# Kernel optimization log

Measured on AMD Instinct MI355X. Metric: run time of the kernel, lower is better.

The kernel has to match this reference:

```python
import jax, jax.numpy as jnp
import numpy as np

DIM = 1024
HEADS = 16
HEAD_DIM = 64
ROT = 32          # rotary_emb_dim = min(max(head_dim//2, 32), head_dim)
BASE = 10000.0
SEQ = 2048
BATCH = 2


def setup_inputs() -> dict:
    key = jax.random.key(0)
    k1, k2, k3, k4 = jax.random.split(key, 4)
    s = 0.02
    return {
        "x": jax.random.normal(k1, (BATCH, SEQ, DIM), dtype=jnp.float32),
        # Linear weights stored as [in, out] (equivalent to torch W^T)
        "w_q": jax.random.normal(k2, (DIM, HEADS * HEAD_DIM), dtype=jnp.float32) * s,
        "w_kv": jax.random.normal(k3, (DIM, 2 * HEADS * HEAD_DIM), dtype=jnp.float32) * s,
        "w_out": jax.random.normal(k4, (HEADS * HEAD_DIM, DIM), dtype=jnp.float32) * s,
    }


def _rotate_half(t):
    # x-transformers style: split last dim in half, (-x2, x1)
    x1, x2 = t[..., : ROT // 2], t[..., ROT // 2 :]
    return jnp.concatenate([-x2, x1], axis=-1)


def _apply_rope(t, cos, sin):
    # rotate only the first ROT dims of head_dim, pass through the rest
    t_rot, t_pass = t[..., :ROT], t[..., ROT:]
    t_rot = t_rot * cos + _rotate_half(t_rot) * sin
    return jnp.concatenate([t_rot, t_pass], axis=-1)


def reference(x, w_q, w_kv, w_out):
    b, n, _ = x.shape
    # QKV projections
    q = (x @ w_q).reshape(b, n, HEADS, HEAD_DIM).transpose(0, 2, 1, 3)  # b h n d
    k, v = jnp.split(x @ w_kv, 2, axis=-1)
    k = k.reshape(b, n, HEADS, HEAD_DIM).transpose(0, 2, 1, 3)
    v = v.reshape(b, n, HEADS, HEAD_DIM).transpose(0, 2, 1, 3)

    # rotary embedding over full kv length (no cache -> k.shape[-2] == n)
    inv_freq = 1.0 / (BASE ** (jnp.arange(0, ROT, 2, dtype=jnp.float32) / ROT))
    freqs = jnp.arange(n, dtype=jnp.float32)[:, None] * inv_freq[None, :]  # [n, ROT/2]
    freqs = jnp.concatenate([freqs, freqs], axis=-1)                        # [n, ROT]
    cos, sin = jnp.cos(freqs), jnp.sin(freqs)
    q = _apply_rope(q, cos, sin)
    k = _apply_rope(k, cos, sin)

    # causal attention
    scale = HEAD_DIM ** -0.5
    scores = jnp.einsum('bhid,bhjd->bhij', q, k) * scale  # [b,h,n,n]
    causal_mask = jnp.tril(jnp.ones((n, n), dtype=bool))
    scores = jnp.where(causal_mask, scores, jnp.finfo(scores.dtype).min)
    attn = jax.nn.softmax(scores, axis=-1)
    out = jnp.einsum('bhij,bhjd->bhid', attn, v)

    out = out.transpose(0, 2, 1, 3).reshape(b, n, HEADS * HEAD_DIM)
    return out @ w_out
```

## Files before the change

kernel.cpp:

```cpp
#include <hip/hip_runtime.h>

typedef unsigned short u16;
typedef unsigned int u32;
typedef __bf16 bf16x8 __attribute__((ext_vector_type(8)));
typedef unsigned short u16x8v __attribute__((ext_vector_type(8)));
typedef unsigned short u16x4v __attribute__((ext_vector_type(4)));
typedef unsigned int u32x4 __attribute__((ext_vector_type(4)));
typedef float f32x4 __attribute__((ext_vector_type(4)));
typedef float f32x16 __attribute__((ext_vector_type(16)));

#define SEQ 2048
#define NH 16
#define HD 64
#define DIMM 1024

__device__ __forceinline__ u16 f2bf(float f) {
  unsigned u = __builtin_bit_cast(unsigned, f);
  u += 0x7fffu + ((u >> 16) & 1u);
  return (u16)(u >> 16);
}
__device__ __forceinline__ float bf2f(u16 b) {
  return __builtin_bit_cast(float, ((unsigned)b) << 16);
}
__device__ __forceinline__ u32 pk2(float a, float b) {
  return (u32)f2bf(a) | ((u32)f2bf(b) << 16);
}

__device__ __forceinline__ void gload16(const u16* g, u16* l) {
  __builtin_amdgcn_global_load_lds(
      (const __attribute__((address_space(1))) unsigned int*)g,
      (__attribute__((address_space(3))) unsigned int*)l, 16, 0, 0);
}

__global__ void conv_x(const float* __restrict__ x, u16* __restrict__ oh) {
  size_t i = (size_t)blockIdx.x * 256 + threadIdx.x;
  f32x4 v = *(const f32x4*)(x + i * 4);
  u16x4v h;
#pragma unroll
  for (int j = 0; j < 4; ++j) h[j] = f2bf(v[j]);
  *(u16x4v*)(oh + i * 4) = h;
}

__global__ void conv_wT(const float* __restrict__ W, u16* __restrict__ Wt,
                        int Kd, int Nd) {
  __shared__ float t[32][33];
  int n0 = blockIdx.x * 32, k0 = blockIdx.y * 32;
  int c = threadIdx.x & 31, r8 = threadIdx.x >> 5;
#pragma unroll
  for (int rr = 0; rr < 32; rr += 8)
    t[r8 + rr][c] = W[(size_t)(k0 + r8 + rr) * Nd + n0 + c];
  __syncthreads();
#pragma unroll
  for (int rr = 0; rr < 32; rr += 8)
    Wt[(size_t)(n0 + r8 + rr) * Kd + k0 + c] = f2bf(t[c][r8 + rr]);
}

__global__ void __launch_bounds__(256, 2)
gemmQKV(const u16* __restrict__ Ah, const u16* __restrict__ Bt,
        u16* __restrict__ Qb, u16* __restrict__ Kb, u16* __restrict__ Vb,
        int M, int N, int K) {
  __shared__ u16 AsH[128][64];
  __shared__ u16 BsH[128][64];
  const int tid = threadIdx.x;
  const int lane = tid & 63, wave = tid >> 6;
  const int wr = wave >> 1, wc = wave & 1;
  const int lr = lane & 15, lg = lane >> 4;
  const int bm = blockIdx.y * 128, bn = blockIdx.x * 128;
  const int lrow = lane >> 3;
  const int lcol8 = (lane & 7) * 8;

  f32x4 acc[4][4];
#pragma unroll
  for (int m = 0; m < 4; ++m)
#pragma unroll
    for (int n = 0; n < 4; ++n) acc[m][n] = (f32x4){0.f, 0.f, 0.f, 0.f};

  for (int k0 = 0; k0 < K; k0 += 64) {
    __syncthreads();
#pragma unroll
    for (int c = 0; c < 4; ++c) {
      int r0 = wave * 32 + c * 8;
      size_t arow = (size_t)(bm + r0 + lrow) * K + k0 + lcol8;
      size_t brow = (size_t)(bn + r0 + lrow) * K + k0 + lcol8;
      gload16(Ah + arow, &AsH[r0][0]);
      gload16(Bt + brow, &BsH[r0][0]);
    }
    __syncthreads();
#pragma unroll
    for (int kk = 0; kk < 2; ++kk) {
      bf16x8 afh[4], bfh[4];
#pragma unroll
      for (int m = 0; m < 4; ++m)
        afh[m] = *(const bf16x8*)&AsH[wr * 64 + m * 16 + lr][kk * 32 + lg * 8];
#pragma unroll
      for (int n = 0; n < 4; ++n)
        bfh[n] = *(const bf16x8*)&BsH[wc * 64 + n * 16 + lr][kk * 32 + lg * 8];
#pragma unroll
      for (int m = 0; m < 4; ++m)
#pragma unroll
        for (int n = 0; n < 4; ++n)
          acc[m][n] = __builtin_amdgcn_mfma_f32_16x16x32_bf16(afh[m], bfh[n],
                                                              acc[m][n], 0, 0, 0);
    }
  }

  const int sel = bn >> 10;
  u16* __restrict__ dst = sel == 0 ? Qb : (sel == 1 ? Kb : Vb);
  if (sel < 2) {
    float inv = __expf(-(float)lr * 0.5756462732485115f);
#pragma unroll
    for (int m = 0; m < 4; ++m) {
#pragma unroll
      for (int r = 0; r < 4; ++r) {
        int row = bm + wr * 64 + m * 16 + 4 * lg + r;
        int s = row & (SEQ - 1);
        float ang = (float)s * inv;
        float sn, cs;
        __sincosf(ang, &sn, &cs);
        float x1 = acc[m][0][r], x2 = acc[m][1][r];
        acc[m][0][r] = x1 * cs - x2 * sn;
        acc[m][1][r] = x2 * cs + x1 * sn;
      }
    }
  }

#pragma unroll
  for (int m = 0; m < 4; ++m) {
#pragma unroll
    for (int n = 0; n < 4; ++n) {
#pragma unroll
      for (int r = 0; r < 4; ++r) {
        int row = bm + wr * 64 + m * 16 + 4 * lg + r;
        int col = bn + wc * 64 + n * 16 + lr;
        int b = row >> 11, s = row & 2047;
        int h = (col >> 6) & 15, d = col & 63;
        dst[(((size_t)(b * NH + h)) * SEQ + s) * HD + d] = f2bf(acc[m][n][r]);
      }
    }
  }
}

__global__ void __launch_bounds__(256, 2)
gemm1(const u16* __restrict__ A, const u16* __restrict__ Bt,
      float* __restrict__ CF, int M, int N, int K) {
  __shared__ u16 As[128][64];
  __shared__ u16 Bs[64][64];
  const int tid = threadIdx.x;
  const int lane = tid & 63, wave = tid >> 6;
  const int wr = wave >> 1, wc = wave & 1;
  const int lr = lane & 15, lg = lane >> 4;
  const int bm = blockIdx.y * 128, bn = blockIdx.x * 64;
  const int lrow = lane >> 3;
  const int lcol8 = (lane & 7) * 8;

  f32x4 acc[4][2];
#pragma unroll
  for (int m = 0; m < 4; ++m)
#pragma unroll
    for (int n = 0; n < 2; ++n) acc[m][n] = (f32x4){0.f, 0.f, 0.f, 0.f};

  for (int k0 = 0; k0 < K; k0 += 64) {
    __syncthreads();
#pragma unroll
    for (int c = 0; c < 4; ++c) {
      int r0 = wave * 32 + c * 8;
      gload16(A + (size_t)(bm + r0 + lrow) * K + k0 + lcol8, &As[r0][0]);
    }
#pragma unroll
    for (int c = 0; c < 2; ++c) {
      int r0 = wave * 16 + c * 8;
      gload16(Bt + (size_t)(bn + r0 + lrow) * K + k0 + lcol8, &Bs[r0][0]);
    }
    __syncthreads();
#pragma unroll
    for (int kk = 0; kk < 2; ++kk) {
      bf16x8 af[4], bfr[2];
#pragma unroll
      for (int m = 0; m < 4; ++m)
        af[m] = *(const bf16x8*)&As[wr * 64 + m * 16 + lr][kk * 32 + lg * 8];
#pragma unroll
      for (int n = 0; n < 2; ++n)
        bfr[n] = *(const bf16x8*)&Bs[wc * 32 + n * 16 + lr][kk * 32 + lg * 8];
#pragma unroll
      for (int m = 0; m < 4; ++m)
#pragma unroll
        for (int n = 0; n < 2; ++n)
          acc[m][n] = __builtin_amdgcn_mfma_f32_16x16x32_bf16(af[m], bfr[n],
                                                              acc[m][n], 0, 0, 0);
    }
  }

#pragma unroll
  for (int m = 0; m < 4; ++m)
#pragma unroll
    for (int n = 0; n < 2; ++n)
#pragma unroll
      for (int r = 0; r < 4; ++r) {
        int row = bm + wr * 64 + m * 16 + 4 * lg + r;
        int col = bn + wc * 32 + n * 16 + lr;
        CF[(size_t)row * N + col] = acc[m][n][r];
      }
}

__global__ void __launch_bounds__(256, 2)
attn_kernel(const u16* __restrict__ Q, const u16* __restrict__ K,
            const u16* __restrict__ V, float* __restrict__ Op0,
            float* __restrict__ Op1, float* __restrict__ ml) {
  __shared__ u16 Ks[64][72];
  __shared__ u16 Vt[64][72];
  const int tid = threadIdx.x, lane = tid & 63, wave = tid >> 6;
  const int hi = lane >> 5, l31 = lane & 31;
  const int bx = blockIdx.x, bh = blockIdx.y;
  const size_t kvbase = (size_t)bh * SEQ * HD;
  const int HS = 32 * SEQ;
  const int kr0 = tid >> 3, kc0 = (tid & 7) * 8;
  const int vr = tid & 63;
  const int vc0A = (tid >> 6) * 8, vc0B = vc0A + 32;

  u16x8v kreg0, kreg1, vreg0, vreg1;

#pragma unroll 1
  for (int phase = 0; phase < 2; ++phase) {
    const int qt = phase ? 15 - bx : bx;
    const int g = phase;
    const int nper = qt + 1;
    const int ktbegin = g * nper;
    const int qrow = qt * 128 + wave * 32 + l31;
    float* __restrict__ Opart = g ? Op1 : Op0;

    const u16* qp = Q + kvbase + (size_t)qrow * HD + 8 * hi;
    bf16x8 qf0 = *(const bf16x8*)(qp);
    bf16x8 qf1 = *(const bf16x8*)(qp + 16);
    bf16x8 qf2 = *(const bf16x8*)(qp + 32);
    bf16x8 qf3 = *(const bf16x8*)(qp + 48);

    f32x16 o0 = {0.f}, o1 = {0.f};
    float m = -1e30f, l = 0.f;

    {
      const u16* kp = K + kvbase + (size_t)(ktbegin * 64) * HD;
      const u16* vp = V + kvbase + (size_t)(ktbegin * 64) * HD;
      kreg0 = *(const u16x8v*)(kp + (size_t)kr0 * HD + kc0);
      kreg1 = *(const u16x8v*)(kp + (size_t)(kr0 + 32) * HD + kc0);
      vreg0 = *(const u16x8v*)(vp + (size_t)vr * HD + vc0A);
      vreg1 = *(const u16x8v*)(vp + (size_t)vr * HD + vc0B);
    }

#pragma unroll 1
    for (int i = 0; i < nper; ++i) {
      const int kt = ktbegin + i;
      __syncthreads();
      *(u16x8v*)&Ks[kr0][kc0] = kreg0;
      *(u16x8v*)&Ks[kr0 + 32][kc0] = kreg1;
#pragma unroll
      for (int j = 0; j < 8; ++j) Vt[vc0A + j][vr] = vreg0[j];
#pragma unroll
      for (int j = 0; j < 8; ++j) Vt[vc0B + j][vr] = vreg1[j];
      __syncthreads();
      if (i + 1 < nper) {
        const u16* kp = K + kvbase + (size_t)((kt + 1) * 64) * HD;
        const u16* vp = V + kvbase + (size_t)((kt + 1) * 64) * HD;
        kreg0 = *(const u16x8v*)(kp + (size_t)kr0 * HD + kc0);
        kreg1 = *(const u16x8v*)(kp + (size_t)(kr0 + 32) * HD + kc0);
        vreg0 = *(const u16x8v*)(vp + (size_t)vr * HD + vc0A);
        vreg1 = *(const u16x8v*)(vp + (size_t)vr * HD + vc0B);
      }

      f32x16 s0 = {0.f}, s1 = {0.f};
      __builtin_amdgcn_s_setprio(1);
#pragma unroll
      for (int kk = 0; kk < 4; ++kk) {
        bf16x8 qk = kk == 0 ? qf0 : (kk == 1 ? qf1 : (kk == 2 ? qf2 : qf3));
        bf16x8 af0 = *(const bf16x8*)&Ks[l31][16 * kk + 8 * hi];
        bf16x8 af1 = *(const bf16x8*)&Ks[32 + l31][16 * kk + 8 * hi];
        s0 = __builtin_amdgcn_mfma_f32_32x32x16_bf16(af0, qk, s0, 0, 0, 0);
        s1 = __builtin_amdgcn_mfma_f32_32x32x16_bf16(af1, qk, s1, 0, 0, 0);
      }
      __builtin_amdgcn_s_setprio(0);
      s0 *= 0.125f;
      s1 *= 0.125f;

      if (kt >= 2 * qt) {
#pragma unroll
        for (int r = 0; r < 16; ++r) {
          int rowi = (r & 3) + 8 * (r >> 2) + 4 * hi;
          if (kt * 64 + rowi > qrow) s0[r] = -1e30f;
          if (kt * 64 + 32 + rowi > qrow) s1[r] = -1e30f;
        }
      }

      float mx = s0[0];
#pragma unroll
      for (int r = 1; r < 16; ++r) mx = fmaxf(mx, s0[r]);
#pragma unroll
      for (int r = 0; r < 16; ++r) mx = fmaxf(mx, s1[r]);
      mx = fmaxf(mx, __shfl_xor(mx, 32));

      bool defer = __all(mx - m <= 8.f);
      if (!defer) {
        float mn = fmaxf(m, mx);
        float fac = __expf(m - mn);
        m = mn;
        l *= fac;
        o0 *= fac;
        o1 *= fac;
      }
      float rsum = 0.f;
#pragma unroll
      for (int r = 0; r < 16; ++r) {
        s0[r] = __expf(s0[r] - m);
        rsum += s0[r];
      }
#pragma unroll
      for (int r = 0; r < 16; ++r) {
        s1[r] = __expf(s1[r] - m);
        rsum += s1[r];
      }
      rsum += __shfl_xor(rsum, 32);
      l += rsum;

      u32 P0a[4], P1a[4], P0b[4], P1b[4];
#pragma unroll
      for (int gg = 0; gg < 4; ++gg) {
        P0a[gg] = pk2(s0[4 * gg], s0[4 * gg + 1]);
        P1a[gg] = pk2(s0[4 * gg + 2], s0[4 * gg + 3]);
        P0b[gg] = pk2(s1[4 * gg], s1[4 * gg + 1]);
        P1b[gg] = pk2(s1[4 * gg + 2], s1[4 * gg + 3]);
      }

      __builtin_amdgcn_s_setprio(1);
#pragma unroll
      for (int c = 0; c < 4; ++c) {
        const int gA = 2 * (c & 1);
        u32 p0lo, p0hi, p1lo, p1hi;
        if (c < 2) {
          p0lo = P0a[gA];
          p0hi = P0a[gA + 1];
          p1lo = P1a[gA];
          p1hi = P1a[gA + 1];
        } else {
          p0lo = P0b[gA];
          p0hi = P0b[gA + 1];
          p1lo = P1b[gA];
          p1hi = P1b[gA + 1];
        }
        u32 send0 = hi ? p0lo : p0hi;
        u32 send1 = hi ? p1lo : p1hi;
        u32 recv0 = (u32)__shfl_xor((int)send0, 32);
        u32 recv1 = (u32)__shfl_xor((int)send1, 32);
        u32 own0 = hi ? p0hi : p0lo;
        u32 own1 = hi ? p1hi : p1lo;
        u32x4 bw;
        bw[0] = hi ? recv0 : own0;
        bw[1] = hi ? recv1 : own1;
        bw[2] = hi ? own0 : recv0;
        bw[3] = hi ? own1 : recv1;
        bf16x8 bfrag = __builtin_bit_cast(bf16x8, bw);
        bf16x8 av0 = *(const bf16x8*)&Vt[l31][16 * c + 8 * hi];
        bf16x8 av1 = *(const bf16x8*)&Vt[32 + l31][16 * c + 8 * hi];
        o0 = __builtin_amdgcn_mfma_f32_32x32x16_bf16(av0, bfrag, o0, 0, 0, 0);
        o1 = __builtin_amdgcn_mfma_f32_32x32x16_bf16(av1, bfrag, o1, 0, 0, 0);
      }
      __builtin_amdgcn_s_setprio(0);
    }

    {
      size_t base = ((size_t)bh * SEQ + qrow) * HD;
#pragma unroll
      for (int gg = 0; gg < 4; ++gg) {
        f32x4 v0 = {o0[4 * gg], o0[4 * gg + 1], o0[4 * gg + 2], o0[4 * gg + 3]};
        f32x4 v1 = {o1[4 * gg], o1[4 * gg + 1], o1[4 * gg + 2], o1[4 * gg + 3]};
        *(f32x4*)(Opart + base + 8 * gg + 4 * hi) = v0;
        *(f32x4*)(Opart + base + 32 + 8 * gg + 4 * hi) = v1;
      }
      if (hi == 0) {
        ml[g * HS + bh * SEQ + qrow] = m;
        ml[2 * HS + g * HS + bh * SEQ + qrow] = l;
      }
    }
    __syncthreads();
  }
}

__global__ void merge_kernel(const float* __restrict__ Op0,
                             const float* __restrict__ Op1,
                             const float* __restrict__ ml,
                             u16* __restrict__ O) {
  int i = blockIdx.x * 256 + threadIdx.x;
  int row = i >> 4;
  int d0 = (i & 15) * 4;
  size_t base = (size_t)row * 64 + d0;
  f32x4 o1 = *(const f32x4*)(Op0 + base);
  f32x4 o2 = *(const f32x4*)(Op1 + base);
  const int HS = 32 * SEQ;
  float m1 = ml[row], m2 = ml[HS + row];
  float l1 = ml[2 * HS + row], l2 = ml[3 * HS + row];
  float M = fmaxf(m1, m2);
  float w1 = __expf(m1 - M), w2 = __expf(m2 - M);
  float inv = 1.0f / (l1 * w1 + l2 * w2);
  int bh = row >> 11, s = row & 2047;
  int b = bh >> 4, h = bh & 15;
  u16x4v rr;
#pragma unroll
  for (int j = 0; j < 4; ++j) rr[j] = f2bf((o1[j] * w1 + o2[j] * w2) * inv);
  *(u16x4v*)(O + ((size_t)(b * SEQ + s)) * DIMM + h * HD + d0) = rr;
}

extern "C" void kernel_launch(void* const* d_in, const int* in_sizes, int n_in,
                              void* d_out, int out_size, void* d_ws, size_t ws_size,
                              hipStream_t stream) {
  const float* x = (const float*)d_in[0];
  const float* wq = (const float*)d_in[1];
  const float* wkv = (const float*)d_in[2];
  const float* wout = (const float*)d_in[3];
  float* out = (float*)d_out;

  u16* ws = (u16*)d_ws;
  const size_t M1 = (size_t)1024 * 1024;
  u16* xh = ws;
  u16* xl = xh + 4 * M1;
  u16* wqTh = xl + 4 * M1;
  u16* wkvTh = wqTh + M1;
  u16* Qb = wkvTh + 2 * M1;
  u16* Kb = Qb + 4 * M1;
  u16* Vb = Kb + 4 * M1;
  float* Op0 = out;
  float* Op1 = (float*)xh;
  float* mlbuf = (float*)wqTh;
  u16* Ob = Qb;
  u16* woutT = Kb;

  conv_x<<<4096, 256, 0, stream>>>(x, xh);
  conv_wT<<<dim3(32, 32), 256, 0, stream>>>(wq, wqTh, 1024, 1024);
  conv_wT<<<dim3(64, 32), 256, 0, stream>>>(wkv, wkvTh, 1024, 2048);

  gemmQKV<<<dim3(24, 32), 256, 0, stream>>>(xh, wqTh, Qb, Kb, Vb,
                                            4096, 3072, 1024);

  attn_kernel<<<dim3(16, 32), 256, 0, stream>>>(Qb, Kb, Vb, Op0, Op1, mlbuf);
  merge_kernel<<<4096, 256, 0, stream>>>(Op0, Op1, mlbuf, Ob);

  conv_wT<<<dim3(32, 32), 256, 0, stream>>>(wout, woutT, 1024, 1024);
  gemm1<<<dim3(16, 32), 256, 0, stream>>>(Ob, woutT, out, 4096, 1024, 1024);
}
```

Baseline: 124.6 us.

## Pre-transpose V and load K/V fragments directly from global memory in attention

Adds a separate kernel that writes V transposed to a [d, seq] layout. The attention kernel then drops its shared-memory K/V staging and both per-tile barriers, and each wave loads its MFMA operand fragments straight from global memory (through cache). The aim is to remove the LDS transposes and block-wide synchronisation. In exchange there is an extra kernel launch, an extra workspace buffer, redundant global loads across the four waves, and no explicit prefetch, so load latency is exposed.

```diff
diff --git a/kernel.cpp b/kernel.cpp
--- a/kernel.cpp
+++ b/kernel.cpp
@@ -53,6 +53,32 @@
 #pragma unroll
   for (int rr = 0; rr < 32; rr += 8)
     Wt[(size_t)(n0 + r8 + rr) * Kd + k0 + c] = f2bf(t[c][r8 + rr]);
+}
+
+__global__ void vT_kernel(const u16* __restrict__ V, u16* __restrict__ Vt) {
+  __shared__ u16 t[64][68];
+  const int tid = threadIdx.x;
+  const int s0 = blockIdx.x * 64;
+  const int bh = blockIdx.y;
+  const size_t base = (size_t)bh * SEQ * HD;
+#pragma unroll
+  for (int it = 0; it < 4; ++it) {
+    int idx = it * 256 + tid;
+    int r = idx >> 4, c4 = (idx & 15) * 4;
+    *(u16x4v*)&t[r][c4] = *(const u16x4v*)(V + base + (size_t)(s0 + r) * HD + c4);
+  }
+  __syncthreads();
+#pragma unroll
+  for (int it = 0; it < 4; ++it) {
+    int idx = it * 256 + tid;
+    int d = idx >> 4, c4 = (idx & 15) * 4;
+    u16x4v v;
+    v[0] = t[c4][d];
+    v[1] = t[c4 + 1][d];
+    v[2] = t[c4 + 2][d];
+    v[3] = t[c4 + 3][d];
+    *(u16x4v*)(Vt + base + (size_t)d * SEQ + s0 + c4) = v;
+  }
 }
 
 __global__ void __launch_bounds__(256, 2)
@@ -204,20 +230,18 @@
 
 __global__ void __launch_bounds__(256, 2)
 attn_kernel(const u16* __restrict__ Q, const u16* __restrict__ K,
-            const u16* __restrict__ V, float* __restrict__ Op0,
+            const u16* __restrict__ Vt, float* __restrict__ Op0,
             float* __restrict__ Op1, float* __restrict__ ml) {
-  __shared__ u16 Ks[64][72];
-  __shared__ u16 Vt[64][72];
   const int tid = threadIdx.x, lane = tid & 63, wave = tid >> 6;
   const int hi = lane >> 5, l31 = lane & 31;
   const int bx = blockIdx.x, bh = blockIdx.y;
   const size_t kvbase = (size_t)bh * SEQ * HD;
   const int HS = 32 * SEQ;
-  const int kr0 = tid >> 3, kc0 = (tid & 7) * 8;
-  const int vr = tid & 63;
-  const int vc0A = (tid >> 6) * 8, vc0B = vc0A + 32;
-
-  u16x8v kreg0, kreg1, vreg0, vreg1;
+
+  const u16* kbase0 = K + kvbase + (size_t)l31 * HD + 8 * hi;
+  const u16* kbase1 = K + kvbase + (size_t)(32 + l31) * HD + 8 * hi;
+  const u16* vbase0 = Vt + kvbase + (size_t)l31 * SEQ + 8 * hi;
+  const u16* vbase1 = Vt + kvbase + (size_t)(32 + l31) * SEQ + 8 * hi;
 
 #pragma unroll 1
   for (int phase = 0; phase < 2; ++phase) {
@@ -237,48 +261,37 @@
     f32x16 o0 = {0.f}, o1 = {0.f};
     float m = -1e30f, l = 0.f;
 
-    {
-      const u16* kp = K + kvbase + (size_t)(ktbegin * 64) * HD;
-      const u16* vp = V + kvbase + (size_t)(ktbegin * 64) * HD;
-      kreg0 = *(const u16x8v*)(kp + (size_t)kr0 * HD + kc0);
-      kreg1 = *(const u16x8v*)(kp + (size_t)(kr0 + 32) * HD + kc0);
-      vreg0 = *(const u16x8v*)(vp + (size_t)vr * HD + vc0A);
-      vreg1 = *(const u16x8v*)(vp + (size_t)vr * HD + vc0B);
-    }
-
 #pragma unroll 1
     for (int i = 0; i < nper; ++i) {
       const int kt = ktbegin + i;
-      __syncthreads();
-      *(u16x8v*)&Ks[kr0][kc0] = kreg0;
-      *(u16x8v*)&Ks[kr0 + 32][kc0] = kreg1;
-#pragma unroll
-      for (int j = 0; j < 8; ++j) Vt[vc0A + j][vr] = vreg0[j];
-#pragma unroll
-      for (int j = 0; j < 8; ++j) Vt[vc0B + j][vr] = vreg1[j];
-      __syncthreads();
-      if (i + 1 < nper) {
-        const u16* kp = K + kvbase + (size_t)((kt + 1) * 64) * HD;
-        const u16* vp = V + kvbase + (size_t)((kt + 1) * 64) * HD;
-        kreg0 = *(const u16x8v*)(kp + (size_t)kr0 * HD + kc0);
-        kreg1 = *(const u16x8v*)(kp + (size_t)(kr0 + 32) * HD + kc0);
-        vreg0 = *(const u16x8v*)(vp + (size_t)vr * HD + vc0A);
-        vreg1 = *(const u16x8v*)(vp + (size_t)vr * HD + vc0B);
-      }
-
+      const u16* kp0 = kbase0 + (size_t)kt * 64 * HD;
+      const u16* kp1 = kbase1 + (size_t)kt * 64 * HD;
+      bf16x8 af0[4], af1[4];
+#pragma unroll
+      for (int kk = 0; kk < 4; ++kk) {
+        af0[kk] = *(const bf16x8*)(kp0 + 16 * kk);
+        af1[kk] = *(const bf16x8*)(kp1 + 16 * kk);
+      }
       f32x16 s0 = {0.f}, s1 = {0.f};
       __builtin_amdgcn_s_setprio(1);
 #pragma unroll
       for (int kk = 0; kk < 4; ++kk) {
         bf16x8 qk = kk == 0 ? qf0 : (kk == 1 ? qf1 : (kk == 2 ? qf2 : qf3));
-        bf16x8 af0 = *(const bf16x8*)&Ks[l31][16 * kk + 8 * hi];
-        bf16x8 af1 = *(const bf16x8*)&Ks[32 + l31][16 * kk + 8 * hi];
-        s0 = __builtin_amdgcn_mfma_f32_32x32x16_bf16(af0, qk, s0, 0, 0, 0);
-        s1 = __builtin_amdgcn_mfma_f32_32x32x16_bf16(af1, qk, s1, 0, 0, 0);
+        s0 = __builtin_amdgcn_mfma_f32_32x32x16_bf16(af0[kk], qk, s0, 0, 0, 0);
+        s1 = __builtin_amdgcn_mfma_f32_32x32x16_bf16(af1[kk], qk, s1, 0, 0, 0);
       }
       __builtin_amdgcn_s_setprio(0);
       s0 *= 0.125f;
       s1 *= 0.125f;
+
+      const u16* vp0 = vbase0 + kt * 64;
+      const u16* vp1 = vbase1 + kt * 64;
+      bf16x8 av0[4], av1[4];
+#pragma unroll
+      for (int c = 0; c < 4; ++c) {
+        av0[c] = *(const bf16x8*)(vp0 + 16 * c);
+        av1[c] = *(const bf16x8*)(vp1 + 16 * c);
+      }
 
       if (kt >= 2 * qt) {
 #pragma unroll
@@ -356,10 +369,8 @@
         bw[2] = hi ? own0 : recv0;
         bw[3] = hi ? own1 : recv1;
         bf16x8 bfrag = __builtin_bit_cast(bf16x8, bw);
-        bf16x8 av0 = *(const bf16x8*)&Vt[l31][16 * c + 8 * hi];
-        bf16x8 av1 = *(const bf16x8*)&Vt[32 + l31][16 * c + 8 * hi];
-        o0 = __builtin_amdgcn_mfma_f32_32x32x16_bf16(av0, bfrag, o0, 0, 0, 0);
-        o1 = __builtin_amdgcn_mfma_f32_32x32x16_bf16(av1, bfrag, o1, 0, 0, 0);
+        o0 = __builtin_amdgcn_mfma_f32_32x32x16_bf16(av0[c], bfrag, o0, 0, 0, 0);
+        o1 = __builtin_amdgcn_mfma_f32_32x32x16_bf16(av1[c], bfrag, o1, 0, 0, 0);
       }
       __builtin_amdgcn_s_setprio(0);
     }
@@ -378,7 +389,6 @@
         ml[2 * HS + g * HS + bh * SEQ + qrow] = l;
       }
     }
-    __syncthreads();
   }
 }
 
@@ -424,6 +434,7 @@
   u16* Qb = wkvTh + 2 * M1;
   u16* Kb = Qb + 4 * M1;
   u16* Vb = Kb + 4 * M1;
+  u16* VTb = Vb + 4 * M1;
   float* Op0 = out;
   float* Op1 = (float*)xh;
   float* mlbuf = (float*)wqTh;
@@ -437,7 +448,9 @@
   gemmQKV<<<dim3(24, 32), 256, 0, stream>>>(xh, wqTh, Qb, Kb, Vb,
                                             4096, 3072, 1024);
 
-  attn_kernel<<<dim3(16, 32), 256, 0, stream>>>(Qb, Kb, Vb, Op0, Op1, mlbuf);
+  vT_kernel<<<dim3(32, 32), 256, 0, stream>>>(Vb, VTb);
+
+  attn_kernel<<<dim3(16, 32), 256, 0, stream>>>(Qb, Kb, VTb, Op0, Op1, mlbuf);
   merge_kernel<<<4096, 256, 0, stream>>>(Op0, Op1, mlbuf, Ob);
 
   conv_wT<<<dim3(32, 32), 256, 0, stream>>>(wout, woutT, 1024, 1024);
```

Result: slower. 153.8 us (+23.4%).

## Double-buffer K/V shared tiles in attention to drop one barrier per iteration

Applied to the files above, without the earlier changes.

Turns the single K and transposed-V LDS tiles into double buffers. The next tile is written into the alternate buffer while the current tile is consumed, and register prefetch now runs two tiles ahead. This cuts the loop from two block barriers per iteration to one, at the cost of doubling LDS use, which may limit occupancy at two blocks per CU.

```diff
diff --git a/kernel.cpp b/kernel.cpp
--- a/kernel.cpp
+++ b/kernel.cpp
@@ -206,8 +206,8 @@
 attn_kernel(const u16* __restrict__ Q, const u16* __restrict__ K,
             const u16* __restrict__ V, float* __restrict__ Op0,
             float* __restrict__ Op1, float* __restrict__ ml) {
-  __shared__ u16 Ks[64][72];
-  __shared__ u16 Vt[64][72];
+  __shared__ u16 Ks[2][64][72];
+  __shared__ u16 Vt[2][64][72];
   const int tid = threadIdx.x, lane = tid & 63, wave = tid >> 6;
   const int hi = lane >> 5, l31 = lane & 31;
   const int bx = blockIdx.x, bh = blockIdx.y;
@@ -245,25 +245,42 @@
       vreg0 = *(const u16x8v*)(vp + (size_t)vr * HD + vc0A);
       vreg1 = *(const u16x8v*)(vp + (size_t)vr * HD + vc0B);
     }
+    *(u16x8v*)&Ks[0][kr0][kc0] = kreg0;
+    *(u16x8v*)&Ks[0][kr0 + 32][kc0] = kreg1;
+#pragma unroll
+    for (int j = 0; j < 8; ++j) Vt[0][vc0A + j][vr] = vreg0[j];
+#pragma unroll
+    for (int j = 0; j < 8; ++j) Vt[0][vc0B + j][vr] = vreg1[j];
+    if (nper > 1) {
+      const u16* kp = K + kvbase + (size_t)((ktbegin + 1) * 64) * HD;
+      const u16* vp = V + kvbase + (size_t)((ktbegin + 1) * 64) * HD;
+      kreg0 = *(const u16x8v*)(kp + (size_t)kr0 * HD + kc0);
+      kreg1 = *(const u16x8v*)(kp + (size_t)(kr0 + 32) * HD + kc0);
+      vreg0 = *(const u16x8v*)(vp + (size_t)vr * HD + vc0A);
+      vreg1 = *(const u16x8v*)(vp + (size_t)vr * HD + vc0B);
+    }
+    __syncthreads();
 
 #pragma unroll 1
     for (int i = 0; i < nper; ++i) {
       const int kt = ktbegin + i;
-      __syncthreads();
-      *(u16x8v*)&Ks[kr0][kc0] = kreg0;
-      *(u16x8v*)&Ks[kr0 + 32][kc0] = kreg1;
-#pragma unroll
-      for (int j = 0; j < 8; ++j) Vt[vc0A + j][vr] = vreg0[j];
-#pragma unroll
-      for (int j = 0; j < 8; ++j) Vt[vc0B + j][vr] = vreg1[j];
-      __syncthreads();
+      const int cur = i & 1;
       if (i + 1 < nper) {
-        const u16* kp = K + kvbase + (size_t)((kt + 1) * 64) * HD;
-        const u16* vp = V + kvbase + (size_t)((kt + 1) * 64) * HD;
-        kreg0 = *(const u16x8v*)(kp + (size_t)kr0 * HD + kc0);
-        kreg1 = *(const u16x8v*)(kp + (size_t)(kr0 + 32) * HD + kc0);
-        vreg0 = *(const u16x8v*)(vp + (size_t)vr * HD + vc0A);
-        vreg1 = *(const u16x8v*)(vp + (size_t)vr * HD + vc0B);
+        const int nxt = cur ^ 1;
+        *(u16x8v*)&Ks[nxt][kr0][kc0] = kreg0;
+        *(u16x8v*)&Ks[nxt][kr0 + 32][kc0] = kreg1;
+#pragma unroll
+        for (int j = 0; j < 8; ++j) Vt[nxt][vc0A + j][vr] = vreg0[j];
+#pragma unroll
+        for (int j = 0; j < 8; ++j) Vt[nxt][vc0B + j][vr] = vreg1[j];
+        if (i + 2 < nper) {
+          const u16* kp = K + kvbase + (size_t)((kt + 2) * 64) * HD;
+          const u16* vp = V + kvbase + (size_t)((kt + 2) * 64) * HD;
+          kreg0 = *(const u16x8v*)(kp + (size_t)kr0 * HD + kc0);
+          kreg1 = *(const u16x8v*)(kp + (size_t)(kr0 + 32) * HD + kc0);
+          vreg0 = *(const u16x8v*)(vp + (size_t)vr * HD + vc0A);
+          vreg1 = *(const u16x8v*)(vp + (size_t)vr * HD + vc0B);
+        }
       }
 
       f32x16 s0 = {0.f}, s1 = {0.f};
@@ -271,8 +288,8 @@
 #pragma unroll
       for (int kk = 0; kk < 4; ++kk) {
         bf16x8 qk = kk == 0 ? qf0 : (kk == 1 ? qf1 : (kk == 2 ? qf2 : qf3));
-        bf16x8 af0 = *(const bf16x8*)&Ks[l31][16 * kk + 8 * hi];
-        bf16x8 af1 = *(const bf16x8*)&Ks[32 + l31][16 * kk + 8 * hi];
+        bf16x8 af0 = *(const bf16x8*)&Ks[cur][l31][16 * kk + 8 * hi];
+        bf16x8 af1 = *(const bf16x8*)&Ks[cur][32 + l31][16 * kk + 8 * hi];
         s0 = __builtin_amdgcn_mfma_f32_32x32x16_bf16(af0, qk, s0, 0, 0, 0);
         s1 = __builtin_amdgcn_mfma_f32_32x32x16_bf16(af1, qk, s1, 0, 0, 0);
       }
@@ -356,12 +373,13 @@
         bw[2] = hi ? own0 : recv0;
         bw[3] = hi ? own1 : recv1;
         bf16x8 bfrag = __builtin_bit_cast(bf16x8, bw);
-        bf16x8 av0 = *(const bf16x8*)&Vt[l31][16 * c + 8 * hi];
-        bf16x8 av1 = *(const bf16x8*)&Vt[32 + l31][16 * c + 8 * hi];
+        bf16x8 av0 = *(const bf16x8*)&Vt[cur][l31][16 * c + 8 * hi];
+        bf16x8 av1 = *(const bf16x8*)&Vt[cur][32 + l31][16 * c + 8 * hi];
         o0 = __builtin_amdgcn_mfma_f32_32x32x16_bf16(av0, bfrag, o0, 0, 0, 0);
         o1 = __builtin_amdgcn_mfma_f32_32x32x16_bf16(av1, bfrag, o1, 0, 0, 0);
       }
       __builtin_amdgcn_s_setprio(0);
+      __syncthreads();
     }
 
     {
@@ -378,7 +396,6 @@
         ml[2 * HS + g * HS + bh * SEQ + qrow] = l;
       }
     }
-    __syncthreads();
   }
 }
 
```

Measured after the change: 126.1 us. No clear change (+1.2%).

## Split causal attention KV range four ways and store bf16 partials

Applied to the files above, without the earlier changes.

The attention kernel now splits each query tile's KV range into four chunks instead of two, and the grid gains a split dimension. This doubles the block count and evens out the causal work per block, and the occupancy hint is raised to four blocks per CU. Partial outputs are written as bf16 instead of fp32 to cut partial-store and merge traffic. The merge kernel combines four partials with their max/sum statistics. In exchange there is more merge work, extra rounding of the unnormalized partials, and some splits with zero tiles.

```diff
diff --git a/kernel.cpp b/kernel.cpp
--- a/kernel.cpp
+++ b/kernel.cpp
@@ -202,15 +202,16 @@
       }
 }
 
-__global__ void __launch_bounds__(256, 2)
+__global__ void __launch_bounds__(256, 4)
 attn_kernel(const u16* __restrict__ Q, const u16* __restrict__ K,
-            const u16* __restrict__ V, float* __restrict__ Op0,
-            float* __restrict__ Op1, float* __restrict__ ml) {
+            const u16* __restrict__ V, u16* __restrict__ P0,
+            u16* __restrict__ P1, u16* __restrict__ P2, u16* __restrict__ P3,
+            float* __restrict__ ml) {
   __shared__ u16 Ks[64][72];
   __shared__ u16 Vt[64][72];
   const int tid = threadIdx.x, lane = tid & 63, wave = tid >> 6;
   const int hi = lane >> 5, l31 = lane & 31;
-  const int bx = blockIdx.x, bh = blockIdx.y;
+  const int bx = blockIdx.x, gg = blockIdx.y, bh = blockIdx.z;
   const size_t kvbase = (size_t)bh * SEQ * HD;
   const int HS = 32 * SEQ;
   const int kr0 = tid >> 3, kc0 = (tid & 7) * 8;
@@ -222,11 +223,13 @@
 #pragma unroll 1
   for (int phase = 0; phase < 2; ++phase) {
     const int qt = phase ? 15 - bx : bx;
-    const int g = phase;
-    const int nper = qt + 1;
-    const int ktbegin = g * nper;
+    const int j = phase ? 3 - gg : gg;
+    const int T1 = qt + 1;
+    const int ktbegin = (j * T1) >> 1;
+    const int ktend = ((j + 1) * T1) >> 1;
+    const int nper = ktend - ktbegin;
     const int qrow = qt * 128 + wave * 32 + l31;
-    float* __restrict__ Opart = g ? Op1 : Op0;
+    u16* __restrict__ Opart = j == 0 ? P0 : (j == 1 ? P1 : (j == 2 ? P2 : P3));
 
     const u16* qp = Q + kvbase + (size_t)qrow * HD + 8 * hi;
     bf16x8 qf0 = *(const bf16x8*)(qp);
@@ -237,172 +240,186 @@
     f32x16 o0 = {0.f}, o1 = {0.f};
     float m = -1e30f, l = 0.f;
 
-    {
-      const u16* kp = K + kvbase + (size_t)(ktbegin * 64) * HD;
-      const u16* vp = V + kvbase + (size_t)(ktbegin * 64) * HD;
-      kreg0 = *(const u16x8v*)(kp + (size_t)kr0 * HD + kc0);
-      kreg1 = *(const u16x8v*)(kp + (size_t)(kr0 + 32) * HD + kc0);
-      vreg0 = *(const u16x8v*)(vp + (size_t)vr * HD + vc0A);
-      vreg1 = *(const u16x8v*)(vp + (size_t)vr * HD + vc0B);
-    }
-
-#pragma unroll 1
-    for (int i = 0; i < nper; ++i) {
-      const int kt = ktbegin + i;
-      __syncthreads();
-      *(u16x8v*)&Ks[kr0][kc0] = kreg0;
-      *(u16x8v*)&Ks[kr0 + 32][kc0] = kreg1;
-#pragma unroll
-      for (int j = 0; j < 8; ++j) Vt[vc0A + j][vr] = vreg0[j];
-#pragma unroll
-      for (int j = 0; j < 8; ++j) Vt[vc0B + j][vr] = vreg1[j];
-      __syncthreads();
-      if (i + 1 < nper) {
-        const u16* kp = K + kvbase + (size_t)((kt + 1) * 64) * HD;
-        const u16* vp = V + kvbase + (size_t)((kt + 1) * 64) * HD;
+    if (nper > 0) {
+      {
+        const u16* kp = K + kvbase + (size_t)(ktbegin * 64) * HD;
+        const u16* vp = V + kvbase + (size_t)(ktbegin * 64) * HD;
         kreg0 = *(const u16x8v*)(kp + (size_t)kr0 * HD + kc0);
         kreg1 = *(const u16x8v*)(kp + (size_t)(kr0 + 32) * HD + kc0);
         vreg0 = *(const u16x8v*)(vp + (size_t)vr * HD + vc0A);
         vreg1 = *(const u16x8v*)(vp + (size_t)vr * HD + vc0B);
       }
 
-      f32x16 s0 = {0.f}, s1 = {0.f};
-      __builtin_amdgcn_s_setprio(1);
-#pragma unroll
-      for (int kk = 0; kk < 4; ++kk) {
-        bf16x8 qk = kk == 0 ? qf0 : (kk == 1 ? qf1 : (kk == 2 ? qf2 : qf3));
-        bf16x8 af0 = *(const bf16x8*)&Ks[l31][16 * kk + 8 * hi];
-        bf16x8 af1 = *(const bf16x8*)&Ks[32 + l31][16 * kk + 8 * hi];
-        s0 = __builtin_amdgcn_mfma_f32_32x32x16_bf16(af0, qk, s0, 0, 0, 0);
-        s1 = __builtin_amdgcn_mfma_f32_32x32x16_bf16(af1, qk, s1, 0, 0, 0);
-      }
-      __builtin_amdgcn_s_setprio(0);
-      s0 *= 0.125f;
-      s1 *= 0.125f;
-
-      if (kt >= 2 * qt) {
+#pragma unroll 1
+      for (int i = 0; i < nper; ++i) {
+        const int kt = ktbegin + i;
+        __syncthreads();
+        *(u16x8v*)&Ks[kr0][kc0] = kreg0;
+        *(u16x8v*)&Ks[kr0 + 32][kc0] = kreg1;
+#pragma unroll
+        for (int jj = 0; jj < 8; ++jj) Vt[vc0A + jj][vr] = vreg0[jj];
+#pragma unroll
+        for (int jj = 0; jj < 8; ++jj) Vt[vc0B + jj][vr] = vreg1[jj];
+        __syncthreads();
+        if (i + 1 < nper) {
+          const u16* kp = K + kvbase + (size_t)((kt + 1) * 64) * HD;
+          const u16* vp = V + kvbase + (size_t)((kt + 1) * 64) * HD;
+          kreg0 = *(const u16x8v*)(kp + (size_t)kr0 * HD + kc0);
+          kreg1 = *(const u16x8v*)(kp + (size_t)(kr0 + 32) * HD + kc0);
+          vreg0 = *(const u16x8v*)(vp + (size_t)vr * HD + vc0A);
+          vreg1 = *(const u16x8v*)(vp + (size_t)vr * HD + vc0B);
+        }
+
+        f32x16 s0 = {0.f}, s1 = {0.f};
+        __builtin_amdgcn_s_setprio(1);
+#pragma unroll
+        for (int kk = 0; kk < 4; ++kk) {
+          bf16x8 qk = kk == 0 ? qf0 : (kk == 1 ? qf1 : (kk == 2 ? qf2 : qf3));
+          bf16x8 af0 = *(const bf16x8*)&Ks[l31][16 * kk + 8 * hi];
+          bf16x8 af1 = *(const bf16x8*)&Ks[32 + l31][16 * kk + 8 * hi];
+          s0 = __builtin_amdgcn_mfma_f32_32x32x16_bf16(af0, qk, s0, 0, 0, 0);
+          s1 = __builtin_amdgcn_mfma_f32_32x32x16_bf16(af1, qk, s1, 0, 0, 0);
+        }
+        __builtin_amdgcn_s_setprio(0);
+        s0 *= 0.125f;
+        s1 *= 0.125f;
+
+        if (kt >= 2 * qt) {
+#pragma unroll
+          for (int r = 0; r < 16; ++r) {
+            int rowi = (r & 3) + 8 * (r >> 2) + 4 * hi;
+            if (kt * 64 + rowi > qrow) s0[r] = -1e30f;
+            if (kt * 64 + 32 + rowi > qrow) s1[r] = -1e30f;
+          }
+        }
+
+        float mx = s0[0];
+#pragma unroll
+        for (int r = 1; r < 16; ++r) mx = fmaxf(mx, s0[r]);
+#pragma unroll
+        for (int r = 0; r < 16; ++r) mx = fmaxf(mx, s1[r]);
+        mx = fmaxf(mx, __shfl_xor(mx, 32));
+
+        bool defer = __all(mx - m <= 8.f);
+        if (!defer) {
+          float mn = fmaxf(m, mx);
+          float fac = __expf(m - mn);
+          m = mn;
+          l *= fac;
+          o0 *= fac;
+          o1 *= fac;
+        }
+        float rsum = 0.f;
 #pragma unroll
         for (int r = 0; r < 16; ++r) {
-          int rowi = (r & 3) + 8 * (r >> 2) + 4 * hi;
-          if (kt * 64 + rowi > qrow) s0[r] = -1e30f;
-          if (kt * 64 + 32 + rowi > qrow) s1[r] = -1e30f;
-        }
-      }
-
-      float mx = s0[0];
-#pragma unroll
-      for (int r = 1; r < 16; ++r) mx = fmaxf(mx, s0[r]);
-#pragma unroll
-      for (int r = 0; r < 16; ++r) mx = fmaxf(mx, s1[r]);
-      mx = fmaxf(mx, __shfl_xor(mx, 32));
-
-      bool defer = __all(mx - m <= 8.f);
-      if (!defer) {
-        float mn = fmaxf(m, mx);
-        float fac = __expf(m - mn);
-        m = mn;
-        l *= fac;
-        o0 *= fac;
-        o1 *= fac;
-      }
-      float rsum = 0.f;
-#pragma unroll
-      for (int r = 0; r < 16; ++r) {
-        s0[r] = __expf(s0[r] - m);
-        rsum += s0[r];
-      }
-#pragma unroll
-      for (int r = 0; r < 16; ++r) {
-        s1[r] = __expf(s1[r] - m);
-        rsum += s1[r];
-      }
-      rsum += __shfl_xor(rsum, 32);
-      l += rsum;
-
-      u32 P0a[4], P1a[4], P0b[4], P1b[4];
-#pragma unroll
-      for (int gg = 0; gg < 4; ++gg) {
-        P0a[gg] = pk2(s0[4 * gg], s0[4 * gg + 1]);
-        P1a[gg] = pk2(s0[4 * gg + 2], s0[4 * gg + 3]);
-        P0b[gg] = pk2(s1[4 * gg], s1[4 * gg + 1]);
-        P1b[gg] = pk2(s1[4 * gg + 2], s1[4 * gg + 3]);
-      }
-
-      __builtin_amdgcn_s_setprio(1);
-#pragma unroll
-      for (int c = 0; c < 4; ++c) {
-        const int gA = 2 * (c & 1);
-        u32 p0lo, p0hi, p1lo, p1hi;
-        if (c < 2) {
-          p0lo = P0a[gA];
-          p0hi = P0a[gA + 1];
-          p1lo = P1a[gA];
-          p1hi = P1a[gA + 1];
-        } else {
-          p0lo = P0b[gA];
-          p0hi = P0b[gA + 1];
-          p1lo = P1b[gA];
-          p1hi = P1b[gA + 1];
-        }
-        u32 send0 = hi ? p0lo : p0hi;
-        u32 send1 = hi ? p1lo : p1hi;
-        u32 recv0 = (u32)__shfl_xor((int)send0, 32);
-        u32 recv1 = (u32)__shfl_xor((int)send1, 32);
-        u32 own0 = hi ? p0hi : p0lo;
-        u32 own1 = hi ? p1hi : p1lo;
-        u32x4 bw;
-        bw[0] = hi ? recv0 : own0;
-        bw[1] = hi ? recv1 : own1;
-        bw[2] = hi ? own0 : recv0;
-        bw[3] = hi ? own1 : recv1;
-        bf16x8 bfrag = __builtin_bit_cast(bf16x8, bw);
-        bf16x8 av0 = *(const bf16x8*)&Vt[l31][16 * c + 8 * hi];
-        bf16x8 av1 = *(const bf16x8*)&Vt[32 + l31][16 * c + 8 * hi];
-        o0 = __builtin_amdgcn_mfma_f32_32x32x16_bf16(av0, bfrag, o0, 0, 0, 0);
-        o1 = __builtin_amdgcn_mfma_f32_32x32x16_bf16(av1, bfrag, o1, 0, 0, 0);
-      }
-      __builtin_amdgcn_s_setprio(0);
+          s0[r] = __expf(s0[r] - m);
+          rsum += s0[r];
+        }
+#pragma unroll
+        for (int r = 0; r < 16; ++r) {
+          s1[r] = __expf(s1[r] - m);
+          rsum += s1[r];
+        }
+        rsum += __shfl_xor(rsum, 32);
+        l += rsum;
+
+        u32 P0a[4], P1a[4], P0b[4], P1b[4];
+#pragma unroll
+        for (int g4 = 0; g4 < 4; ++g4) {
+          P0a[g4] = pk2(s0[4 * g4], s0[4 * g4 + 1]);
+          P1a[g4] = pk2(s0[4 * g4 + 2], s0[4 * g4 + 3]);
+          P0b[g4] = pk2(s1[4 * g4], s1[4 * g4 + 1]);
+          P1b[g4] = pk2(s1[4 * g4 + 2], s1[4 * g4 + 3]);
+        }
+
+        __builtin_amdgcn_s_setprio(1);
+#pragma unroll
+        for (int c = 0; c < 4; ++c) {
+          const int gA = 2 * (c & 1);
+          u32 p0lo, p0hi, p1lo, p1hi;
+          if (c < 2) {
+            p0lo = P0a[gA];
+            p0hi = P0a[gA + 1];
+            p1lo = P1a[gA];
+            p1hi = P1a[gA + 1];
+          } else {
+            p0lo = P0b[gA];
+            p0hi = P0b[gA + 1];
+            p1lo = P1b[gA];
+            p1hi = P1b[gA + 1];
+          }
+          u32 send0 = hi ? p0lo : p0hi;
+          u32 send1 = hi ? p1lo : p1hi;
+          u32 recv0 = (u32)__shfl_xor((int)send0, 32);
+          u32 recv1 = (u32)__shfl_xor((int)send1, 32);
+          u32 own0 = hi ? p0hi : p0lo;
+          u32 own1 = hi ? p1hi : p1lo;
+          u32x4 bw;
+          bw[0] = hi ? recv0 : own0;
+          bw[1] = hi ? recv1 : own1;
+          bw[2] = hi ? own0 : recv0;
+          bw[3] = hi ? own1 : recv1;
+          bf16x8 bfrag = __builtin_bit_cast(bf16x8, bw);
+          bf16x8 av0 = *(const bf16x8*)&Vt[l31][16 * c + 8 * hi];
+          bf16x8 av1 = *(const bf16x8*)&Vt[32 + l31][16 * c + 8 * hi];
+          o0 = __builtin_amdgcn_mfma_f32_32x32x16_bf16(av0, bfrag, o0, 0, 0, 0);
+          o1 = __builtin_amdgcn_mfma_f32_32x32x16_bf16(av1, bfrag, o1, 0, 0, 0);
+        }
+        __builtin_amdgcn_s_setprio(0);
+      }
     }
 
     {
-      size_t base = ((size_t)bh * SEQ + qrow) * HD;
-#pragma unroll
-      for (int gg = 0; gg < 4; ++gg) {
-        f32x4 v0 = {o0[4 * gg], o0[4 * gg + 1], o0[4 * gg + 2], o0[4 * gg + 3]};
-        f32x4 v1 = {o1[4 * gg], o1[4 * gg + 1], o1[4 * gg + 2], o1[4 * gg + 3]};
-        *(f32x4*)(Opart + base + 8 * gg + 4 * hi) = v0;
-        *(f32x4*)(Opart + base + 32 + 8 * gg + 4 * hi) = v1;
+      size_t obase = ((size_t)bh * SEQ + qrow) * HD;
+#pragma unroll
+      for (int g4 = 0; g4 < 4; ++g4) {
+        u16x4v w0, w1;
+#pragma unroll
+        for (int k = 0; k < 4; ++k) {
+          w0[k] = f2bf(o0[4 * g4 + k]);
+          w1[k] = f2bf(o1[4 * g4 + k]);
+        }
+        *(u16x4v*)(Opart + obase + 8 * g4 + 4 * hi) = w0;
+        *(u16x4v*)(Opart + obase + 32 + 8 * g4 + 4 * hi) = w1;
       }
       if (hi == 0) {
-        ml[g * HS + bh * SEQ + qrow] = m;
-        ml[2 * HS + g * HS + bh * SEQ + qrow] = l;
-      }
-    }
-    __syncthreads();
+        ml[j * HS + bh * SEQ + qrow] = m;
+        ml[4 * HS + j * HS + bh * SEQ + qrow] = l;
+      }
+    }
   }
 }
 
-__global__ void merge_kernel(const float* __restrict__ Op0,
-                             const float* __restrict__ Op1,
+__global__ void merge_kernel(const u16* __restrict__ P0,
+                             const u16* __restrict__ P1,
+                             const u16* __restrict__ P2,
+                             const u16* __restrict__ P3,
                              const float* __restrict__ ml,
                              u16* __restrict__ O) {
   int i = blockIdx.x * 256 + threadIdx.x;
   int row = i >> 4;
   int d0 = (i & 15) * 4;
   size_t base = (size_t)row * 64 + d0;
-  f32x4 o1 = *(const f32x4*)(Op0 + base);
-  f32x4 o2 = *(const f32x4*)(Op1 + base);
   const int HS = 32 * SEQ;
-  float m1 = ml[row], m2 = ml[HS + row];
-  float l1 = ml[2 * HS + row], l2 = ml[3 * HS + row];
-  float M = fmaxf(m1, m2);
-  float w1 = __expf(m1 - M), w2 = __expf(m2 - M);
-  float inv = 1.0f / (l1 * w1 + l2 * w2);
+  float m0 = ml[row], m1 = ml[HS + row], m2 = ml[2 * HS + row],
+        m3 = ml[3 * HS + row];
+  float l0 = ml[4 * HS + row], l1 = ml[5 * HS + row], l2 = ml[6 * HS + row],
+        l3 = ml[7 * HS + row];
+  float M = fmaxf(fmaxf(m0, m1), fmaxf(m2, m3));
+  float w0 = __expf(m0 - M), w1 = __expf(m1 - M), w2 = __expf(m2 - M),
+        w3 = __expf(m3 - M);
+  float inv = 1.0f / (l0 * w0 + l1 * w1 + l2 * w2 + l3 * w3);
+  u16x4v p0 = *(const u16x4v*)(P0 + base);
+  u16x4v p1 = *(const u16x4v*)(P1 + base);
+  u16x4v p2 = *(const u16x4v*)(P2 + base);
+  u16x4v p3 = *(const u16x4v*)(P3 + base);
   int bh = row >> 11, s = row & 2047;
   int b = bh >> 4, h = bh & 15;
   u16x4v rr;
 #pragma unroll
-  for (int j = 0; j < 4; ++j) rr[j] = f2bf((o1[j] * w1 + o2[j] * w2) * inv);
+  for (int k = 0; k < 4; ++k)
+    rr[k] = f2bf((bf2f(p0[k]) * w0 + bf2f(p1[k]) * w1 + bf2f(p2[k]) * w2 +
+                  bf2f(p3[k]) * w3) * inv);
   *(u16x4v*)(O + ((size_t)(b * SEQ + s)) * DIMM + h * HD + d0) = rr;
 }
 
@@ -424,8 +441,10 @@
   u16* Qb = wkvTh + 2 * M1;
   u16* Kb = Qb + 4 * M1;
   u16* Vb = Kb + 4 * M1;
-  float* Op0 = out;
-  float* Op1 = (float*)xh;
+  u16* Pq0 = (u16*)out;
+  u16* Pq1 = (u16*)out + 4 * M1;
+  u16* Pq2 = xh;
+  u16* Pq3 = xl;
   float* mlbuf = (float*)wqTh;
   u16* Ob = Qb;
   u16* woutT = Kb;
@@ -437,8 +456,9 @@
   gemmQKV<<<dim3(24, 32), 256, 0, stream>>>(xh, wqTh, Qb, Kb, Vb,
                                             4096, 3072, 1024);
 
-  attn_kernel<<<dim3(16, 32), 256, 0, stream>>>(Qb, Kb, Vb, Op0, Op1, mlbuf);
-  merge_kernel<<<4096, 256, 0, stream>>>(Op0, Op1, mlbuf, Ob);
+  attn_kernel<<<dim3(16, 2, 32), 256, 0, stream>>>(Qb, Kb, Vb, Pq0, Pq1, Pq2,
+                                                   Pq3, mlbuf);
+  merge_kernel<<<4096, 256, 0, stream>>>(Pq0, Pq1, Pq2, Pq3, mlbuf, Ob);
 
   conv_wT<<<dim3(32, 32), 256, 0, stream>>>(wout, woutT, 1024, 1024);
   gemm1<<<dim3(16, 32), 256, 0, stream>>>(Ob, woutT, out, 4096, 1024, 1024);
```

After: 129.8 us. 1.04x slower.
